# Optimization experiments

Hardware: AMD Instinct MI355X
Metric: run time of the kernel (lower is better)

The kernel has to match this reference:

```python
import jax, jax.numpy as jnp
import numpy as np

NEG_SLOPE = 0.01  # torch F.leaky_relu default


def _mlp_block(x, mask, W, b):
    # x: [B,P,V,F]; mask: [B,P,V] bool; W: [H,F]; b: [H]
    h = jax.nn.leaky_relu(jnp.einsum('bpvf,hf->bpvh', x, W) + b, NEG_SLOPE)
    m = mask[..., None]
    out = jnp.where(m, h, 0.0)                                   # zeros at masked-out slots
    neg = jnp.where(m, out, -jnp.inf)
    pool = jnp.max(neg, axis=2, keepdims=True)                   # [B,P,1,H] masked max-pool
    any_valid = jnp.any(mask, axis=2)[:, :, None, None]
    pool = jnp.where(any_valid, pool, 0.0)                       # fully-masked polylines -> 0
    rep = jnp.broadcast_to(pool, out.shape)
    return jnp.concatenate([out, rep], axis=-1)                  # [B,P,V,2H]


def setup_inputs() -> dict:
    key = jax.random.key(0)
    ks = jax.random.split(key, 8)
    B, P, V, F, H = 32, 512, 32, 16, 64
    input_var = jax.random.normal(ks[0], (B, P, V, F), dtype=jnp.float32)
    input_mask = jax.random.bernoulli(ks[1], 0.8, (B, P, V))
    s = 1.0 / np.sqrt(F)
    W1 = jax.random.uniform(ks[2], (H, F), jnp.float32, -s, s)
    b1 = jax.random.uniform(ks[3], (H,), jnp.float32, -s, s)
    s2 = 1.0 / np.sqrt(2 * H)
    W2 = jax.random.uniform(ks[4], (H, 2 * H), jnp.float32, -s2, s2)
    b2 = jax.random.uniform(ks[5], (H,), jnp.float32, -s2, s2)
    W3 = jax.random.uniform(ks[6], (H, 2 * H), jnp.float32, -s2, s2)
    b3 = jax.random.uniform(ks[7], (H,), jnp.float32, -s2, s2)
    return {"input_var": input_var, "input_mask": input_mask,
            "W1": W1, "b1": b1, "W2": W2, "b2": b2, "W3": W3, "b3": b3,
            "size1": P, "size2": V}


def reference(input_var, input_mask, W1, b1, W2, b2, W3, b3, size1, size2):
    hidden = W1.shape[0]
    x = _mlp_block(input_var, input_mask, W1, b1)
    y = _mlp_block(x, input_mask, W2, b2)
    z = _mlp_block(y, input_mask, W3, b3)
    out = z[:, :, 0, -hidden:]                                   # pooled half, same across V
    out = jnp.where(jnp.any(input_mask, axis=2)[..., None], out, 0.0)
    return out
```

## Files before the change

kernel.cpp:

```cpp
#include <hip/hip_runtime.h>
#include <math.h>

namespace {

typedef _Float16 f16x8 __attribute__((ext_vector_type(8)));
typedef _Float16 f16x2 __attribute__((ext_vector_type(2)));
typedef float    f32x16 __attribute__((ext_vector_type(16)));
typedef unsigned int uint;

__device__ __forceinline__ uint pkrtz(float a, float b) {
    return __builtin_bit_cast(uint, __builtin_amdgcn_cvt_pkrtz(a, b));
}
__device__ __forceinline__ uint pk_add(uint a, uint b) {
    uint r; asm("v_pk_add_f16 %0, %1, %2" : "=v"(r) : "v"(a), "v"(b)); return r;
}
__device__ __forceinline__ uint pk_mul(uint a, uint b) {
    uint r; asm("v_pk_mul_f16 %0, %1, %2" : "=v"(r) : "v"(a), "v"(b)); return r;
}
__device__ __forceinline__ uint pk_max(uint a, uint b) {
    uint r; asm("v_pk_max_f16 %0, %1, %2" : "=v"(r) : "v"(a), "v"(b)); return r;
}

__global__ void prep_pack(const float* __restrict__ W1, const float* __restrict__ W2,
                          const float* __restrict__ W3, const int* __restrict__ M,
                          unsigned short* __restrict__ wsW, uint* __restrict__ wsM)
{
    int t = blockIdx.x * blockDim.x + threadIdx.x;
    if (t < 34 * 64) {
        int f = t >> 6, l = t & 63, nb = l & 31, kg = l >> 5;
        const float* src; int K, ki, nt2;
        if (f < 2)       { src = W1; K = 16;  ki = 0;           nt2 = f; }
        else if (f < 18) { int g = f - 2;  src = W2; K = 128; ki = g >> 1; nt2 = g & 1; }
        else             { int g = f - 18; src = W3; K = 128; ki = g >> 1; nt2 = g & 1; }
        const float* s = src + (size_t)(32 * nt2 + nb) * K + 16 * ki + 8 * kg;
        uint4 q;
        q.x = pkrtz(s[0], s[1]); q.y = pkrtz(s[2], s[3]);
        q.z = pkrtz(s[4], s[5]); q.w = pkrtz(s[6], s[7]);
        *(uint4*)(wsW + (size_t)f * 512 + l * 8) = q;
    } else if (t < 34 * 64 + 16384) {
        int bp = t - 34 * 64;
        const int4* mp = (const int4*)(M + bp * 32);
        uint bits = 0;
        #pragma unroll
        for (int i = 0; i < 8; ++i) {
            int4 v = mp[i];
            bits |= ((v.x ? 1u : 0u) | (v.y ? 2u : 0u) |
                     (v.z ? 4u : 0u) | (v.w ? 8u : 0u)) << (4 * i);
        }
        wsM[bp] = bits;
    }
}

__global__ __launch_bounds__(256, 3) void fused_mlp_v10(
    const float* __restrict__ X, const uint* __restrict__ MPK,
    const unsigned short* __restrict__ WF,
    const float* __restrict__ B1, const float* __restrict__ B2,
    const float* __restrict__ B3, float* __restrict__ OUT)
{
    __shared__ __align__(16) unsigned char sXb[4][2][4096];
    __shared__ __align__(16) _Float16 sP[4][2][64];

    const int t = threadIdx.x, w = t >> 6, l = t & 63;
    const int hb = l >> 5, mtl = (l >> 4) & 1;
    const size_t bp0 = (size_t)blockIdx.x * 8 + w * 2;

    unsigned char* sb[2] = { &sXb[w][0][0], &sXb[w][1][0] };
    _Float16*     pl[2] = { &sP[w][0][0],  &sP[w][1][0]  };

    uint wb0 = (uint)((l & 7) * 32 + mtl * 256 + ((l >> 3) & 1) * 1024 + hb * 8);
    wb0 ^= (uint)(mtl << 5);
    const uint wb1 = (wb0 + 512u) ^ 64u;
    const uint rb = (uint)(mtl * 2048 + hb * 1024 + ((l & 15) >> 1) * 4);
    const uint sel = (l & 1) ? 0x07060302u : 0x05040100u;
    const uint SL2 = pkrtz(0.01f, 0.01f);

    bool anyv[2]; uint adm[2][4][2];
    #pragma unroll
    for (int u = 0; u < 2; ++u) {
        uint mk = MPK[bp0 + u];
        anyv[u] = (mk != 0u);
        #pragma unroll
        for (int g = 0; g < 4; ++g) {
            uint nib = (mk >> (8 * g + 4 * hb)) & 15u;
            adm[u][g][0] = (nib & 1u ? 0u : 0xFC00u) | (nib & 2u ? 0u : 0xFC000000u);
            adm[u][g][1] = (nib & 4u ? 0u : 0xFC00u) | (nib & 8u ? 0u : 0xFC000000u);
        }
    }

    f16x8 a1f[2];
    #pragma unroll
    for (int u = 0; u < 2; ++u) {
        const float4* xp = (const float4*)(X + ((bp0 + u) * 32 + (l & 31)) * 16 + 8 * hb);
        float4 x0 = xp[0], x1 = xp[1];
        uint4 q;
        q.x = pkrtz(x0.x, x0.y); q.y = pkrtz(x0.z, x0.w);
        q.z = pkrtz(x1.x, x1.y); q.w = pkrtz(x1.z, x1.w);
        a1f[u] = __builtin_bit_cast(f16x8, q);
    }

    f32x16 zc;
    #pragma unroll
    for (int i = 0; i < 16; ++i) zc[i] = 0.f;

    f32x16 acc[2][2];

    {
        const _Float16* wp = (const _Float16*)WF + l * 8;
        f16x8 wf0 = *(const f16x8*)wp;
        f16x8 wf1 = *(const f16x8*)(wp + 512);
        #pragma unroll
        for (int u = 0; u < 2; ++u) {
            acc[u][0] = __builtin_amdgcn_mfma_f32_32x32x16_f16(a1f[u], wf0, zc, 0, 0, 0);
            acc[u][1] = __builtin_amdgcn_mfma_f32_32x32x16_f16(a1f[u], wf1, zc, 0, 0, 0);
        }
    }

    auto epi = [&](int u, const float* __restrict__ Bp, bool dostore) {
        unsigned char* sbu = sb[u];
        _Float16* plu = pl[u];
        #pragma unroll
        for (int nt2 = 0; nt2 < 2; ++nt2) {
            float bsc = Bp[32 * nt2 + (l & 31)];
            uint bpk = pkrtz(bsc, bsc);
            uint base = nt2 ? wb1 : wb0;
            uint pp = 0xFC00FC00u;
            #pragma unroll
            for (int g = 0; g < 4; ++g) {
                uint d01 = pkrtz(acc[u][nt2][4 * g + 0], acc[u][nt2][4 * g + 1]);
                uint d23 = pkrtz(acc[u][nt2][4 * g + 2], acc[u][nt2][4 * g + 3]);
                d01 = pk_add(d01, bpk);  d23 = pk_add(d23, bpk);
                d01 = pk_max(d01, pk_mul(d01, SL2));
                d23 = pk_max(d23, pk_mul(d23, SL2));
                if (dostore) {
                    uint2 st; st.x = d01; st.y = d23;
                    *(uint2*)(sbu + base + (g >> 1) * 2048 + (g & 1) * 16) = st;
                }
                pp = pk_max(pp, pk_add(d01, adm[u][g][0]));
                pp = pk_max(pp, pk_add(d23, adm[u][g][1]));
            }
            f16x2 ph = __builtin_bit_cast(f16x2, pp);
            float pv = fmaxf((float)ph[0], (float)ph[1]);
            pv = fmaxf(pv, __shfl_xor(pv, 32));
            pv = anyv[u] ? pv : 0.f;
            if (dostore) {
                if (l < 32) plu[32 * nt2 + (l & 31)] = (_Float16)pv;
            } else {
                if (l < 32) OUT[(bp0 + u) * 64 + 32 * nt2 + (l & 31)] = pv;
            }
        }
    };

    auto layerK = [&](int fb) {
        #pragma unroll
        for (int ki = 0; ki < 8; ++ki) {
            const _Float16* wp = (const _Float16*)WF + (size_t)(fb + 2 * ki) * 512 + l * 8;
            f16x8 wf0 = *(const f16x8*)wp;
            f16x8 wf1 = *(const f16x8*)(wp + 512);
            #pragma unroll
            for (int u = 0; u < 2; ++u) {
                f16x8 a;
                if (ki < 4) {
                    const unsigned char* p = sb[u] + rb + 256 * ki;
                    uint F0 = *(const uint*)(p + 32 * (0 ^ ki));
                    uint F1 = *(const uint*)(p + 32 * (1 ^ ki));
                    uint F2 = *(const uint*)(p + 32 * (2 ^ ki));
                    uint F3 = *(const uint*)(p + 32 * (3 ^ ki));
                    uint F4 = *(const uint*)(p + 32 * (4 ^ ki));
                    uint F5 = *(const uint*)(p + 32 * (5 ^ ki));
                    uint F6 = *(const uint*)(p + 32 * (6 ^ ki));
                    uint F7 = *(const uint*)(p + 32 * (7 ^ ki));
                    uint4 q;
                    q.x = __builtin_amdgcn_perm(F1, F0, sel);
                    q.y = __builtin_amdgcn_perm(F3, F2, sel);
                    q.z = __builtin_amdgcn_perm(F5, F4, sel);
                    q.w = __builtin_amdgcn_perm(F7, F6, sel);
                    a = __builtin_bit_cast(f16x8, q);
                } else {
                    a = *(const f16x8*)(pl[u] + 16 * (ki - 4) + 8 * hb);
                }
                acc[u][0] = __builtin_amdgcn_mfma_f32_32x32x16_f16(
                    a, wf0, ki == 0 ? zc : acc[u][0], 0, 0, 0);
                acc[u][1] = __builtin_amdgcn_mfma_f32_32x32x16_f16(
                    a, wf1, ki == 0 ? zc : acc[u][1], 0, 0, 0);
            }
        }
    };

    epi(0, B1, true);  epi(1, B1, true);
    layerK(2);
    epi(0, B2, true);  epi(1, B2, true);
    layerK(18);
    epi(0, B3, false); epi(1, B3, false);
}
}

extern "C" void kernel_launch(void* const* d_in, const int* in_sizes, int n_in,
                              void* d_out, int out_size, void* d_ws, size_t ws_size,
                              hipStream_t stream) {
    (void)in_sizes; (void)n_in; (void)ws_size; (void)out_size;
    const float* X  = (const float*)d_in[0];
    const int*   M  = (const int*)d_in[1];
    const float* W1 = (const float*)d_in[2];
    const float* B1 = (const float*)d_in[3];
    const float* W2 = (const float*)d_in[4];
    const float* B2 = (const float*)d_in[5];
    const float* W3 = (const float*)d_in[6];
    const float* B3 = (const float*)d_in[7];
    float* OUT = (float*)d_out;

    unsigned short* WF  = (unsigned short*)d_ws;
    uint*           MPK = (uint*)((char*)d_ws + 34816);

    prep_pack<<<(34 * 64 + 16384 + 255) / 256, 256, 0, stream>>>(W1, W2, W3, M, WF, MPK);
    fused_mlp_v10<<<2048, 256, 0, stream>>>(X, MPK, WF, B1, B2, B3, OUT);
}
```

Baseline: 114.8 us.

## Interleave epilogue of one polyline with MFMA of the other and re-swizzle LDS

Restructures each wave's two polylines into a software pipeline. The epilogue (bias, leaky-relu, LDS store, masked max-pool) of one unit is interleaved slice by slice with the MFMA K-loop of the other, so VALU and LDS work can overlap matrix-core work. The LDS write and read addressing also gets an extra XOR swizzle to reduce bank conflicts. This raises register pressure from the extra live accumulators, and the swizzle has to stay consistent between writes and reads.

```diff
diff --git a/kernel.cpp b/kernel.cpp
--- a/kernel.cpp
+++ b/kernel.cpp
@@ -51,7 +51,7 @@
     }
 }
 
-__global__ __launch_bounds__(256, 3) void fused_mlp_v10(
+__global__ __launch_bounds__(256, 3) void fused_mlp_v11(
     const float* __restrict__ X, const uint* __restrict__ MPK,
     const unsigned short* __restrict__ WF,
     const float* __restrict__ B1, const float* __restrict__ B2,
@@ -61,16 +61,18 @@
     __shared__ __align__(16) _Float16 sP[4][2][64];
 
     const int t = threadIdx.x, w = t >> 6, l = t & 63;
-    const int hb = l >> 5, mtl = (l >> 4) & 1;
+    const int hb = l >> 5, mtl = (l >> 4) & 1, l3 = (l >> 3) & 1;
     const size_t bp0 = (size_t)blockIdx.x * 8 + w * 2;
 
     unsigned char* sb[2] = { &sXb[w][0][0], &sXb[w][1][0] };
     _Float16*     pl[2] = { &sP[w][0][0],  &sP[w][1][0]  };
 
-    uint wb0 = (uint)((l & 7) * 32 + mtl * 256 + ((l >> 3) & 1) * 1024 + hb * 8);
-    wb0 ^= (uint)(mtl << 5);
+    uint wb0 = (uint)((l & 7) * 32 + mtl * 256 + l3 * 1024 + hb * 8);
+    wb0 ^= (uint)((mtl << 5) ^ (l3 << 4));
     const uint wb1 = (wb0 + 512u) ^ 64u;
-    const uint rb = (uint)(mtl * 2048 + hb * 1024 + ((l & 15) >> 1) * 4);
+    uint rbA = (uint)(mtl * 2048 + hb * 1024 + ((l & 15) >> 1) * 4);
+    rbA ^= (uint)((hb << 4) ^ (mtl << 5));
+    const uint rbB = rbA ^ 32u;
     const uint sel = (l & 1) ? 0x07060302u : 0x05040100u;
     const uint SL2 = pkrtz(0.01f, 0.01f);
 
@@ -108,89 +110,103 @@
         const _Float16* wp = (const _Float16*)WF + l * 8;
         f16x8 wf0 = *(const f16x8*)wp;
         f16x8 wf1 = *(const f16x8*)(wp + 512);
-        #pragma unroll
-        for (int u = 0; u < 2; ++u) {
-            acc[u][0] = __builtin_amdgcn_mfma_f32_32x32x16_f16(a1f[u], wf0, zc, 0, 0, 0);
-            acc[u][1] = __builtin_amdgcn_mfma_f32_32x32x16_f16(a1f[u], wf1, zc, 0, 0, 0);
-        }
-    }
-
-    auto epi = [&](int u, const float* __restrict__ Bp, bool dostore) {
-        unsigned char* sbu = sb[u];
-        _Float16* plu = pl[u];
+        acc[0][0] = __builtin_amdgcn_mfma_f32_32x32x16_f16(a1f[0], wf0, zc, 0, 0, 0);
+        acc[0][1] = __builtin_amdgcn_mfma_f32_32x32x16_f16(a1f[0], wf1, zc, 0, 0, 0);
+        acc[1][0] = __builtin_amdgcn_mfma_f32_32x32x16_f16(a1f[1], wf0, zc, 0, 0, 0);
+        acc[1][1] = __builtin_amdgcn_mfma_f32_32x32x16_f16(a1f[1], wf1, zc, 0, 0, 0);
+    }
+
+    auto epi_slice = [&](int ue, int s, uint bpk0, uint bpk1,
+                         uint& pp0, uint& pp1, bool dostore) {
+        const int nt2 = s >> 2, g = s & 3;
+        const f32x16& A = acc[ue][nt2];
+        uint bpk = nt2 ? bpk1 : bpk0;
+        uint d01 = pk_add(pkrtz(A[4 * g + 0], A[4 * g + 1]), bpk);
+        uint d23 = pk_add(pkrtz(A[4 * g + 2], A[4 * g + 3]), bpk);
+        d01 = pk_max(d01, pk_mul(d01, SL2));
+        d23 = pk_max(d23, pk_mul(d23, SL2));
+        if (dostore) {
+            uint wba = ((nt2 ? wb1 : wb0)
+                        ^ (uint)(((g & 1) << 4) ^ ((g >> 1) << 5)))
+                       + (uint)((g >> 1) * 2048);
+            uint2 st; st.x = d01; st.y = d23;
+            *(uint2*)(sb[ue] + wba) = st;
+        }
+        uint& pp = nt2 ? pp1 : pp0;
+        pp = pk_max(pp, pk_add(d01, adm[ue][g][0]));
+        pp = pk_max(pp, pk_add(d23, adm[ue][g][1]));
+    };
+
+    auto epi_fin = [&](int ue, uint pp0, uint pp1, bool dostore) {
         #pragma unroll
         for (int nt2 = 0; nt2 < 2; ++nt2) {
-            float bsc = Bp[32 * nt2 + (l & 31)];
-            uint bpk = pkrtz(bsc, bsc);
-            uint base = nt2 ? wb1 : wb0;
-            uint pp = 0xFC00FC00u;
-            #pragma unroll
-            for (int g = 0; g < 4; ++g) {
-                uint d01 = pkrtz(acc[u][nt2][4 * g + 0], acc[u][nt2][4 * g + 1]);
-                uint d23 = pkrtz(acc[u][nt2][4 * g + 2], acc[u][nt2][4 * g + 3]);
-                d01 = pk_add(d01, bpk);  d23 = pk_add(d23, bpk);
-                d01 = pk_max(d01, pk_mul(d01, SL2));
-                d23 = pk_max(d23, pk_mul(d23, SL2));
-                if (dostore) {
-                    uint2 st; st.x = d01; st.y = d23;
-                    *(uint2*)(sbu + base + (g >> 1) * 2048 + (g & 1) * 16) = st;
-                }
-                pp = pk_max(pp, pk_add(d01, adm[u][g][0]));
-                pp = pk_max(pp, pk_add(d23, adm[u][g][1]));
-            }
-            f16x2 ph = __builtin_bit_cast(f16x2, pp);
+            f16x2 ph = __builtin_bit_cast(f16x2, nt2 ? pp1 : pp0);
             float pv = fmaxf((float)ph[0], (float)ph[1]);
             pv = fmaxf(pv, __shfl_xor(pv, 32));
-            pv = anyv[u] ? pv : 0.f;
+            pv = anyv[ue] ? pv : 0.f;
             if (dostore) {
-                if (l < 32) plu[32 * nt2 + (l & 31)] = (_Float16)pv;
+                if (l < 32) pl[ue][32 * nt2 + (l & 31)] = (_Float16)pv;
             } else {
-                if (l < 32) OUT[(bp0 + u) * 64 + 32 * nt2 + (l & 31)] = pv;
+                if (l < 32) OUT[(bp0 + ue) * 64 + 32 * nt2 + (l & 31)] = pv;
             }
         }
     };
 
-    auto layerK = [&](int fb) {
+    auto epi_full = [&](int ue, const float* __restrict__ Bp, bool dostore) {
+        uint pp0 = 0xFC00FC00u, pp1 = 0xFC00FC00u;
+        float b0 = Bp[l & 31], b1 = Bp[32 + (l & 31)];
+        uint bpk0 = pkrtz(b0, b0), bpk1 = pkrtz(b1, b1);
+        #pragma unroll
+        for (int s = 0; s < 8; ++s)
+            epi_slice(ue, s, bpk0, bpk1, pp0, pp1, dostore);
+        epi_fin(ue, pp0, pp1, dostore);
+    };
+
+    auto fused_step = [&](int uk, int fb, int ue, const float* __restrict__ Bp,
+                          bool store_epi) {
+        uint pp0 = 0xFC00FC00u, pp1 = 0xFC00FC00u;
+        float b0 = Bp[l & 31], b1 = Bp[32 + (l & 31)];
+        uint bpk0 = pkrtz(b0, b0), bpk1 = pkrtz(b1, b1);
+        const unsigned char* pA = sb[uk] + rbA;
+        const unsigned char* pB = sb[uk] + rbB;
+        f32x16 na0, na1;
         #pragma unroll
         for (int ki = 0; ki < 8; ++ki) {
             const _Float16* wp = (const _Float16*)WF + (size_t)(fb + 2 * ki) * 512 + l * 8;
             f16x8 wf0 = *(const f16x8*)wp;
             f16x8 wf1 = *(const f16x8*)(wp + 512);
-            #pragma unroll
-            for (int u = 0; u < 2; ++u) {
-                f16x8 a;
-                if (ki < 4) {
-                    const unsigned char* p = sb[u] + rb + 256 * ki;
-                    uint F0 = *(const uint*)(p + 32 * (0 ^ ki));
-                    uint F1 = *(const uint*)(p + 32 * (1 ^ ki));
-                    uint F2 = *(const uint*)(p + 32 * (2 ^ ki));
-                    uint F3 = *(const uint*)(p + 32 * (3 ^ ki));
-                    uint F4 = *(const uint*)(p + 32 * (4 ^ ki));
-                    uint F5 = *(const uint*)(p + 32 * (5 ^ ki));
-                    uint F6 = *(const uint*)(p + 32 * (6 ^ ki));
-                    uint F7 = *(const uint*)(p + 32 * (7 ^ ki));
-                    uint4 q;
-                    q.x = __builtin_amdgcn_perm(F1, F0, sel);
-                    q.y = __builtin_amdgcn_perm(F3, F2, sel);
-                    q.z = __builtin_amdgcn_perm(F5, F4, sel);
-                    q.w = __builtin_amdgcn_perm(F7, F6, sel);
-                    a = __builtin_bit_cast(f16x8, q);
-                } else {
-                    a = *(const f16x8*)(pl[u] + 16 * (ki - 4) + 8 * hb);
+            f16x8 a;
+            if (ki < 4) {
+                uint F[8];
+                #pragma unroll
+                for (int j = 0; j < 8; ++j) {
+                    const int e = j ^ ki;
+                    const uint off = (uint)(256 * ki + 32 * (e & ~1));
+                    F[j] = *(const uint*)(((e & 1) ? pB : pA) + off);
                 }
-                acc[u][0] = __builtin_amdgcn_mfma_f32_32x32x16_f16(
-                    a, wf0, ki == 0 ? zc : acc[u][0], 0, 0, 0);
-                acc[u][1] = __builtin_amdgcn_mfma_f32_32x32x16_f16(
-                    a, wf1, ki == 0 ? zc : acc[u][1], 0, 0, 0);
+                uint4 q;
+                q.x = __builtin_amdgcn_perm(F[1], F[0], sel);
+                q.y = __builtin_amdgcn_perm(F[3], F[2], sel);
+                q.z = __builtin_amdgcn_perm(F[5], F[4], sel);
+                q.w = __builtin_amdgcn_perm(F[7], F[6], sel);
+                a = __builtin_bit_cast(f16x8, q);
+            } else {
+                a = *(const f16x8*)(pl[uk] + 16 * (ki - 4) + 8 * hb);
             }
-        }
-    };
-
-    epi(0, B1, true);  epi(1, B1, true);
-    layerK(2);
-    epi(0, B2, true);  epi(1, B2, true);
-    layerK(18);
-    epi(0, B3, false); epi(1, B3, false);
+            na0 = __builtin_amdgcn_mfma_f32_32x32x16_f16(a, wf0, ki ? na0 : zc, 0, 0, 0);
+            na1 = __builtin_amdgcn_mfma_f32_32x32x16_f16(a, wf1, ki ? na1 : zc, 0, 0, 0);
+            epi_slice(ue, ki, bpk0, bpk1, pp0, pp1, store_epi);
+        }
+        epi_fin(ue, pp0, pp1, store_epi);
+        acc[uk][0] = na0; acc[uk][1] = na1;
+    };
+
+    epi_full(0, B1, true);
+    fused_step(0, 2,  1, B1, true);
+    fused_step(1, 2,  0, B2, true);
+    fused_step(0, 18, 1, B2, true);
+    fused_step(1, 18, 0, B3, false);
+    epi_full(1, B3, false);
 }
 }
 
@@ -212,5 +228,5 @@
     uint*           MPK = (uint*)((char*)d_ws + 34816);
 
     prep_pack<<<(34 * 64 + 16384 + 255) / 256, 256, 0, stream>>>(W1, W2, W3, M, WF, MPK);
-    fused_mlp_v10<<<2048, 256, 0, stream>>>(X, MPK, WF, B1, B2, B3, OUT);
-}
+    fused_mlp_v11<<<2048, 256, 0, stream>>>(X, MPK, WF, B1, B2, B3, OUT);
+}
```

Result: no change. 114.6 us (-0.2%).

## Transpose MFMA operands to keep activations in registers, drop shared memory

Applied to the files above, without the earlier changes.

Swaps the MFMA operand roles so weights become the A operand and activations the B operand. Each wave's accumulator output then maps directly onto the next layer's input fragment through cross-half shuffles, so the LDS staging buffers and permute-based reloads go away. Bias is folded into the MFMA initial accumulator instead of being added in packed f16. The masked max-pool now uses a 5-step shuffle reduction across vertices. Each wave handles one polyline instead of two, with twice as many blocks. The trade is many more cross-lane shuffles per epilogue and less per-wave instruction-level parallelism between the two independent MFMA chains.

```diff
diff --git a/kernel.cpp b/kernel.cpp
--- a/kernel.cpp
+++ b/kernel.cpp
@@ -51,146 +51,128 @@
     }
 }
 
-__global__ __launch_bounds__(256, 3) void fused_mlp_v10(
+__global__ __launch_bounds__(256, 3) void fused_mlp_v12(
     const float* __restrict__ X, const uint* __restrict__ MPK,
     const unsigned short* __restrict__ WF,
     const float* __restrict__ B1, const float* __restrict__ B2,
     const float* __restrict__ B3, float* __restrict__ OUT)
 {
-    __shared__ __align__(16) unsigned char sXb[4][2][4096];
-    __shared__ __align__(16) _Float16 sP[4][2][64];
+    const int t = threadIdx.x, w = t >> 6, l = t & 63;
+    const int vr = l & 31, hb = l >> 5;
+    const size_t bp = (size_t)blockIdx.x * 4 + w;
 
-    const int t = threadIdx.x, w = t >> 6, l = t & 63;
-    const int hb = l >> 5, mtl = (l >> 4) & 1;
-    const size_t bp0 = (size_t)blockIdx.x * 8 + w * 2;
-
-    unsigned char* sb[2] = { &sXb[w][0][0], &sXb[w][1][0] };
-    _Float16*     pl[2] = { &sP[w][0][0],  &sP[w][1][0]  };
-
-    uint wb0 = (uint)((l & 7) * 32 + mtl * 256 + ((l >> 3) & 1) * 1024 + hb * 8);
-    wb0 ^= (uint)(mtl << 5);
-    const uint wb1 = (wb0 + 512u) ^ 64u;
-    const uint rb = (uint)(mtl * 2048 + hb * 1024 + ((l & 15) >> 1) * 4);
-    const uint sel = (l & 1) ? 0x07060302u : 0x05040100u;
     const uint SL2 = pkrtz(0.01f, 0.01f);
 
-    bool anyv[2]; uint adm[2][4][2];
-    #pragma unroll
-    for (int u = 0; u < 2; ++u) {
-        uint mk = MPK[bp0 + u];
-        anyv[u] = (mk != 0u);
-        #pragma unroll
-        for (int g = 0; g < 4; ++g) {
-            uint nib = (mk >> (8 * g + 4 * hb)) & 15u;
-            adm[u][g][0] = (nib & 1u ? 0u : 0xFC00u) | (nib & 2u ? 0u : 0xFC000000u);
-            adm[u][g][1] = (nib & 4u ? 0u : 0xFC00u) | (nib & 8u ? 0u : 0xFC000000u);
-        }
-    }
+    const uint mk = MPK[bp];
+    const bool anyv = (mk != 0u);
+    const uint adm = ((mk >> vr) & 1u) ? 0u : 0xFC00FC00u;
 
-    f16x8 a1f[2];
-    #pragma unroll
-    for (int u = 0; u < 2; ++u) {
-        const float4* xp = (const float4*)(X + ((bp0 + u) * 32 + (l & 31)) * 16 + 8 * hb);
+    f16x8 bfx;
+    {
+        const float4* xp = (const float4*)(X + ((size_t)bp * 32 + vr) * 16 + 8 * hb);
         float4 x0 = xp[0], x1 = xp[1];
         uint4 q;
         q.x = pkrtz(x0.x, x0.y); q.y = pkrtz(x0.z, x0.w);
         q.z = pkrtz(x1.x, x1.y); q.w = pkrtz(x1.z, x1.w);
-        a1f[u] = __builtin_bit_cast(f16x8, q);
+        bfx = __builtin_bit_cast(f16x8, q);
     }
 
-    f32x16 zc;
-    #pragma unroll
-    for (int i = 0; i < 16; ++i) zc[i] = 0.f;
+    auto buildC = [&](const float* __restrict__ Bp, int n2) -> f32x16 {
+        f32x16 cc;
+        #pragma unroll
+        for (int r = 0; r < 16; ++r) {
+            int base = (r & 3) + 8 * (r >> 2) + 32 * n2;
+            cc[r] = hb ? Bp[base + 4] : Bp[base];
+        }
+        return cc;
+    };
 
-    f32x16 acc[2][2];
+    auto red5 = [&](uint v) -> uint {
+        v = pk_max(v, (uint)__shfl_xor((int)v, 1));
+        v = pk_max(v, (uint)__shfl_xor((int)v, 2));
+        v = pk_max(v, (uint)__shfl_xor((int)v, 4));
+        v = pk_max(v, (uint)__shfl_xor((int)v, 8));
+        v = pk_max(v, (uint)__shfl_xor((int)v, 16));
+        return v;
+    };
+
+    f32x16 acc0, acc1;
+    uint P[2][4][2];
+    uint PL[2][4][2];
+
+    auto epilogue = [&]() {
+        #pragma unroll
+        for (int n2 = 0; n2 < 2; ++n2) {
+            #pragma unroll
+            for (int g = 0; g < 4; ++g)
+                #pragma unroll
+                for (int b = 0; b < 2; ++b) {
+                    const f32x16& A = n2 ? acc1 : acc0;
+                    uint d = pkrtz(A[4 * g + 2 * b], A[4 * g + 2 * b + 1]);
+                    d = pk_max(d, pk_mul(d, SL2));
+                    P[n2][g][b] = d;
+                    uint m = red5(pk_add(d, adm));
+                    PL[n2][g][b] = anyv ? m : 0u;
+                }
+        }
+    };
+
+    auto layerK = [&](int fb, const float* __restrict__ Bp) {
+        f32x16 cb0 = buildC(Bp, 0), cb1 = buildC(Bp, 1);
+        f32x16 a0, a1;
+        #pragma unroll
+        for (int s = 0; s < 8; ++s) {
+            const uint (&S)[2][4][2] = (s < 4) ? P : PL;
+            const int p = s & 3, n2s = p >> 1, sg = p & 1;
+            uint s00 = S[n2s][2 * sg + 0][0], s01 = S[n2s][2 * sg + 0][1];
+            uint s10 = S[n2s][2 * sg + 1][0], s11 = S[n2s][2 * sg + 1][1];
+            uint w0 = (uint)__shfl_xor((int)s00, 32);
+            uint w1 = (uint)__shfl_xor((int)s01, 32);
+            uint w2 = (uint)__shfl_xor((int)s10, 32);
+            uint w3 = (uint)__shfl_xor((int)s11, 32);
+            uint4 q;
+            q.x = hb ? w2 : s00;
+            q.y = hb ? w3 : s01;
+            q.z = hb ? s10 : w0;
+            q.w = hb ? s11 : w1;
+            f16x8 bf = __builtin_bit_cast(f16x8, q);
+            const _Float16* wp = (const _Float16*)WF + (size_t)(fb + 2 * s) * 512 + l * 8;
+            f16x8 wA0 = *(const f16x8*)wp;
+            f16x8 wA1 = *(const f16x8*)(wp + 512);
+            a0 = __builtin_amdgcn_mfma_f32_32x32x16_f16(wA0, bf, s ? a0 : cb0, 0, 0, 0);
+            a1 = __builtin_amdgcn_mfma_f32_32x32x16_f16(wA1, bf, s ? a1 : cb1, 0, 0, 0);
+        }
+        acc0 = a0; acc1 = a1;
+    };
 
     {
         const _Float16* wp = (const _Float16*)WF + l * 8;
-        f16x8 wf0 = *(const f16x8*)wp;
-        f16x8 wf1 = *(const f16x8*)(wp + 512);
-        #pragma unroll
-        for (int u = 0; u < 2; ++u) {
-            acc[u][0] = __builtin_amdgcn_mfma_f32_32x32x16_f16(a1f[u], wf0, zc, 0, 0, 0);
-            acc[u][1] = __builtin_amdgcn_mfma_f32_32x32x16_f16(a1f[u], wf1, zc, 0, 0, 0);
-        }
+        f16x8 wA0 = *(const f16x8*)wp;
+        f16x8 wA1 = *(const f16x8*)(wp + 512);
+        f32x16 cb0 = buildC(B1, 0), cb1 = buildC(B1, 1);
+        acc0 = __builtin_amdgcn_mfma_f32_32x32x16_f16(wA0, bfx, cb0, 0, 0, 0);
+        acc1 = __builtin_amdgcn_mfma_f32_32x32x16_f16(wA1, bfx, cb1, 0, 0, 0);
     }
 
-    auto epi = [&](int u, const float* __restrict__ Bp, bool dostore) {
-        unsigned char* sbu = sb[u];
-        _Float16* plu = pl[u];
+    epilogue();
+    layerK(2, B2);
+    epilogue();
+    layerK(18, B3);
+    epilogue();
+
+    if (vr == 0) {
+        float* o = OUT + bp * 64 + 4 * hb;
         #pragma unroll
-        for (int nt2 = 0; nt2 < 2; ++nt2) {
-            float bsc = Bp[32 * nt2 + (l & 31)];
-            uint bpk = pkrtz(bsc, bsc);
-            uint base = nt2 ? wb1 : wb0;
-            uint pp = 0xFC00FC00u;
+        for (int n2 = 0; n2 < 2; ++n2)
             #pragma unroll
-            for (int g = 0; g < 4; ++g) {
-                uint d01 = pkrtz(acc[u][nt2][4 * g + 0], acc[u][nt2][4 * g + 1]);
-                uint d23 = pkrtz(acc[u][nt2][4 * g + 2], acc[u][nt2][4 * g + 3]);
-                d01 = pk_add(d01, bpk);  d23 = pk_add(d23, bpk);
-                d01 = pk_max(d01, pk_mul(d01, SL2));
-                d23 = pk_max(d23, pk_mul(d23, SL2));
-                if (dostore) {
-                    uint2 st; st.x = d01; st.y = d23;
-                    *(uint2*)(sbu + base + (g >> 1) * 2048 + (g & 1) * 16) = st;
+            for (int g = 0; g < 4; ++g)
+                #pragma unroll
+                for (int b = 0; b < 2; ++b) {
+                    f16x2 h2 = __builtin_bit_cast(f16x2, PL[n2][g][b]);
+                    float2 st; st.x = (float)h2[0]; st.y = (float)h2[1];
+                    *(float2*)(o + 32 * n2 + 8 * g + 2 * b) = st;
                 }
-                pp = pk_max(pp, pk_add(d01, adm[u][g][0]));
-                pp = pk_max(pp, pk_add(d23, adm[u][g][1]));
-            }
-            f16x2 ph = __builtin_bit_cast(f16x2, pp);
-            float pv = fmaxf((float)ph[0], (float)ph[1]);
-            pv = fmaxf(pv, __shfl_xor(pv, 32));
-            pv = anyv[u] ? pv : 0.f;
-            if (dostore) {
-                if (l < 32) plu[32 * nt2 + (l & 31)] = (_Float16)pv;
-            } else {
-                if (l < 32) OUT[(bp0 + u) * 64 + 32 * nt2 + (l & 31)] = pv;
-            }
-        }
-    };
-
-    auto layerK = [&](int fb) {
-        #pragma unroll
-        for (int ki = 0; ki < 8; ++ki) {
-            const _Float16* wp = (const _Float16*)WF + (size_t)(fb + 2 * ki) * 512 + l * 8;
-            f16x8 wf0 = *(const f16x8*)wp;
-            f16x8 wf1 = *(const f16x8*)(wp + 512);
-            #pragma unroll
-            for (int u = 0; u < 2; ++u) {
-                f16x8 a;
-                if (ki < 4) {
-                    const unsigned char* p = sb[u] + rb + 256 * ki;
-                    uint F0 = *(const uint*)(p + 32 * (0 ^ ki));
-                    uint F1 = *(const uint*)(p + 32 * (1 ^ ki));
-                    uint F2 = *(const uint*)(p + 32 * (2 ^ ki));
-                    uint F3 = *(const uint*)(p + 32 * (3 ^ ki));
-                    uint F4 = *(const uint*)(p + 32 * (4 ^ ki));
-                    uint F5 = *(const uint*)(p + 32 * (5 ^ ki));
-                    uint F6 = *(const uint*)(p + 32 * (6 ^ ki));
-                    uint F7 = *(const uint*)(p + 32 * (7 ^ ki));
-                    uint4 q;
-                    q.x = __builtin_amdgcn_perm(F1, F0, sel);
-                    q.y = __builtin_amdgcn_perm(F3, F2, sel);
-                    q.z = __builtin_amdgcn_perm(F5, F4, sel);
-                    q.w = __builtin_amdgcn_perm(F7, F6, sel);
-                    a = __builtin_bit_cast(f16x8, q);
-                } else {
-                    a = *(const f16x8*)(pl[u] + 16 * (ki - 4) + 8 * hb);
-                }
-                acc[u][0] = __builtin_amdgcn_mfma_f32_32x32x16_f16(
-                    a, wf0, ki == 0 ? zc : acc[u][0], 0, 0, 0);
-                acc[u][1] = __builtin_amdgcn_mfma_f32_32x32x16_f16(
-                    a, wf1, ki == 0 ? zc : acc[u][1], 0, 0, 0);
-            }
-        }
-    };
-
-    epi(0, B1, true);  epi(1, B1, true);
-    layerK(2);
-    epi(0, B2, true);  epi(1, B2, true);
-    layerK(18);
-    epi(0, B3, false); epi(1, B3, false);
+    }
 }
 }
 
@@ -212,5 +194,5 @@
     uint*           MPK = (uint*)((char*)d_ws + 34816);
 
     prep_pack<<<(34 * 64 + 16384 + 255) / 256, 256, 0, stream>>>(W1, W2, W3, M, WF, MPK);
-    fused_mlp_v10<<<2048, 256, 0, stream>>>(X, MPK, WF, B1, B2, B3, OUT);
+    fused_mlp_v12<<<4096, 256, 0, stream>>>(X, MPK, WF, B1, B2, B3, OUT);
 }
```

Measured after the change: 144.4 us. +25.8%, slower.

## Fold weight conversion and mask bit-packing into fused kernel, drop prep launch

Applied to the files above, without the earlier changes.

Removes the separate prep kernel that converted weights to fp16 fragments and packed masks into bitfields. The main kernel now reads fp32 weights directly and converts them per wave with cvt_pkrtz, and builds each polyline's mask bits from 32 wave-uniform scalar loads. This removes one kernel launch and its serialization, but repeats the weight conversion in every wave and issues more global loads.

```diff
diff --git a/kernel.cpp b/kernel.cpp
--- a/kernel.cpp
+++ b/kernel.cpp
@@ -21,41 +21,12 @@
     uint r; asm("v_pk_max_f16 %0, %1, %2" : "=v"(r) : "v"(a), "v"(b)); return r;
 }
 
-__global__ void prep_pack(const float* __restrict__ W1, const float* __restrict__ W2,
-                          const float* __restrict__ W3, const int* __restrict__ M,
-                          unsigned short* __restrict__ wsW, uint* __restrict__ wsM)
-{
-    int t = blockIdx.x * blockDim.x + threadIdx.x;
-    if (t < 34 * 64) {
-        int f = t >> 6, l = t & 63, nb = l & 31, kg = l >> 5;
-        const float* src; int K, ki, nt2;
-        if (f < 2)       { src = W1; K = 16;  ki = 0;           nt2 = f; }
-        else if (f < 18) { int g = f - 2;  src = W2; K = 128; ki = g >> 1; nt2 = g & 1; }
-        else             { int g = f - 18; src = W3; K = 128; ki = g >> 1; nt2 = g & 1; }
-        const float* s = src + (size_t)(32 * nt2 + nb) * K + 16 * ki + 8 * kg;
-        uint4 q;
-        q.x = pkrtz(s[0], s[1]); q.y = pkrtz(s[2], s[3]);
-        q.z = pkrtz(s[4], s[5]); q.w = pkrtz(s[6], s[7]);
-        *(uint4*)(wsW + (size_t)f * 512 + l * 8) = q;
-    } else if (t < 34 * 64 + 16384) {
-        int bp = t - 34 * 64;
-        const int4* mp = (const int4*)(M + bp * 32);
-        uint bits = 0;
-        #pragma unroll
-        for (int i = 0; i < 8; ++i) {
-            int4 v = mp[i];
-            bits |= ((v.x ? 1u : 0u) | (v.y ? 2u : 0u) |
-                     (v.z ? 4u : 0u) | (v.w ? 8u : 0u)) << (4 * i);
-        }
-        wsM[bp] = bits;
-    }
-}
-
-__global__ __launch_bounds__(256, 3) void fused_mlp_v10(
-    const float* __restrict__ X, const uint* __restrict__ MPK,
-    const unsigned short* __restrict__ WF,
-    const float* __restrict__ B1, const float* __restrict__ B2,
-    const float* __restrict__ B3, float* __restrict__ OUT)
+__global__ __launch_bounds__(256, 3) void fused_mlp_v15(
+    const float* __restrict__ X, const int* __restrict__ M,
+    const float* __restrict__ W1, const float* __restrict__ B1,
+    const float* __restrict__ W2, const float* __restrict__ B2,
+    const float* __restrict__ W3, const float* __restrict__ B3,
+    float* __restrict__ OUT)
 {
     __shared__ __align__(16) unsigned char sXb[4][2][4096];
     __shared__ __align__(16) _Float16 sP[4][2][64];
@@ -77,7 +48,11 @@
     bool anyv[2]; uint adm[2][4][2];
     #pragma unroll
     for (int u = 0; u < 2; ++u) {
-        uint mk = MPK[bp0 + u];
+        const uint* Mu = (const uint*)M
+            + (size_t)__builtin_amdgcn_readfirstlane((uint)(bp0 + u)) * 32;
+        uint mk = 0;
+        #pragma unroll
+        for (int i = 0; i < 32; ++i) mk |= (Mu[i] ? 1u : 0u) << i;
         anyv[u] = (mk != 0u);
         #pragma unroll
         for (int g = 0; g < 4; ++g) {
@@ -86,6 +61,18 @@
             adm[u][g][1] = (nib & 4u ? 0u : 0xFC00u) | (nib & 8u ? 0u : 0xFC000000u);
         }
     }
+
+    auto cvt8 = [&](const float* __restrict__ p) -> f16x8 {
+        float4 f0 = *(const float4*)p;
+        float4 f1 = *(const float4*)(p + 4);
+        uint4 q;
+        q.x = pkrtz(f0.x, f0.y); q.y = pkrtz(f0.z, f0.w);
+        q.z = pkrtz(f1.x, f1.y); q.w = pkrtz(f1.z, f1.w);
+        return __builtin_bit_cast(f16x8, q);
+    };
+    const float* w1b = W1 + (l & 31) * 16  + 8 * hb;
+    const float* w2b = W2 + (l & 31) * 128 + 8 * hb;
+    const float* w3b = W3 + (l & 31) * 128 + 8 * hb;
 
     f16x8 a1f[2];
     #pragma unroll
@@ -105,9 +92,8 @@
     f32x16 acc[2][2];
 
     {
-        const _Float16* wp = (const _Float16*)WF + l * 8;
-        f16x8 wf0 = *(const f16x8*)wp;
-        f16x8 wf1 = *(const f16x8*)(wp + 512);
+        f16x8 wf0 = cvt8(w1b);
+        f16x8 wf1 = cvt8(w1b + 512);
         #pragma unroll
         for (int u = 0; u < 2; ++u) {
             acc[u][0] = __builtin_amdgcn_mfma_f32_32x32x16_f16(a1f[u], wf0, zc, 0, 0, 0);
@@ -150,12 +136,11 @@
         }
     };
 
-    auto layerK = [&](int fb) {
+    auto layerK = [&](const float* __restrict__ wmb) {
         #pragma unroll
         for (int ki = 0; ki < 8; ++ki) {
-            const _Float16* wp = (const _Float16*)WF + (size_t)(fb + 2 * ki) * 512 + l * 8;
-            f16x8 wf0 = *(const f16x8*)wp;
-            f16x8 wf1 = *(const f16x8*)(wp + 512);
+            f16x8 wf0 = cvt8(wmb + ki * 16);
+            f16x8 wf1 = cvt8(wmb + 4096 + ki * 16);
             #pragma unroll
             for (int u = 0; u < 2; ++u) {
                 f16x8 a;
@@ -187,9 +172,9 @@
     };
 
     epi(0, B1, true);  epi(1, B1, true);
-    layerK(2);
+    layerK(w2b);
     epi(0, B2, true);  epi(1, B2, true);
-    layerK(18);
+    layerK(w3b);
     epi(0, B3, false); epi(1, B3, false);
 }
 }
@@ -197,7 +182,7 @@
 extern "C" void kernel_launch(void* const* d_in, const int* in_sizes, int n_in,
                               void* d_out, int out_size, void* d_ws, size_t ws_size,
                               hipStream_t stream) {
-    (void)in_sizes; (void)n_in; (void)ws_size; (void)out_size;
+    (void)in_sizes; (void)n_in; (void)d_ws; (void)ws_size; (void)out_size;
     const float* X  = (const float*)d_in[0];
     const int*   M  = (const int*)d_in[1];
     const float* W1 = (const float*)d_in[2];
@@ -208,9 +193,5 @@
     const float* B3 = (const float*)d_in[7];
     float* OUT = (float*)d_out;
 
-    unsigned short* WF  = (unsigned short*)d_ws;
-    uint*           MPK = (uint*)((char*)d_ws + 34816);
-
-    prep_pack<<<(34 * 64 + 16384 + 255) / 256, 256, 0, stream>>>(W1, W2, W3, M, WF, MPK);
-    fused_mlp_v10<<<2048, 256, 0, stream>>>(X, MPK, WF, B1, B2, B3, OUT);
+    fused_mlp_v15<<<2048, 256, 0, stream>>>(X, M, W1, B1, W2, B2, W3, B3, OUT);
 }
```

Result: slower. 152.0 us (+32.4%).
